# Kernel optimization log

Measured on AMD Instinct MI355X. Metric: run time of the kernel, lower is better.

## Reference

```python
import jax, jax.numpy as jnp
import numpy as np

EPS = 1e-8

def setup_inputs() -> dict:
    key = jax.random.key(0)
    ks = jax.random.split(key, 10)
    B, T, D = 128, 128, 512
    inp = {"joint": jax.random.normal(ks[0], (B, D), dtype=jnp.float32)}
    names = ["f00", "f01", "f02", "f10", "f11", "f12", "f20", "f21", "f22"]
    for n, k in zip(names, ks[1:]):
        inp[n] = jax.random.normal(k, (B, T, D), dtype=jnp.float32)
    inp["B"] = B
    return inp


def reference(joint, f00, f01, f02, f10, f11, f12, f20, f21, f22, B):
    # F: [N, N, B, T, D] with N = 3
    F = jnp.stack([
        jnp.stack([f00, f01, f02]),
        jnp.stack([f10, f11, f12]),
        jnp.stack([f20, f21, f22]),
    ])
    fmean = F.mean(axis=3)                                   # [N, N, B, D]
    num = jnp.einsum("bd,ijbd->ijb", joint, fmean)           # [N, N, B]
    denom = num.sum(axis=1, keepdims=True) + EPS             # [N, 1, B]
    b = num / denom                                          # [N, N, B]
    # intra-scale weighted sum: f_ii[i] = sum_j b[i,j] * F[i,j]
    f_ii = jnp.einsum("ijb,ijbtd->ibtd", b, F)               # [N, B, T, D]
    fii_mean = f_ii.mean(axis=2)                             # [N, B, D]
    num2 = jnp.einsum("bd,ibd->ib", joint, fii_mean)         # [N, B]
    denom2 = num2.sum(axis=0) + EPS                          # [B]
    lam = num2 / denom2                                      # [N, B]
    return jnp.einsum("ib,ibd->bd", lam, fii_mean)           # [B, D]
```

## Files before the change

### kernel.cpp

```cpp
#include <hip/hip_runtime.h>

#define EPS 1e-8f

namespace {
constexpr int Bc = 128;
constexpr int Tc = 128;
constexpr int Dc = 512;
constexpr int D4 = Dc / 4;
constexpr int THREADS = 256;
constexpr int BLOCKS_PER_TENSOR = (Bc * D4) / THREADS;
}

__global__ __launch_bounds__(256) void hm_mean_kernel(
    const float* __restrict__ f0, const float* __restrict__ f1,
    const float* __restrict__ f2, const float* __restrict__ f3,
    const float* __restrict__ f4, const float* __restrict__ f5,
    const float* __restrict__ f6, const float* __restrict__ f7,
    const float* __restrict__ f8, float* __restrict__ fmean)
{
    const float* fs[9] = {f0, f1, f2, f3, f4, f5, f6, f7, f8};
    const int q   = blockIdx.x / BLOCKS_PER_TENSOR;
    const int idx = (blockIdx.x % BLOCKS_PER_TENSOR) * THREADS + threadIdx.x;
    const int b   = idx >> 7;
    const int d4  = idx & (D4 - 1);

    const float4* src = reinterpret_cast<const float4*>(fs[q]) + (size_t)b * Tc * D4 + d4;

    float4 a0 = make_float4(0.f, 0.f, 0.f, 0.f);
    float4 a1 = make_float4(0.f, 0.f, 0.f, 0.f);
    #pragma unroll 8
    for (int t = 0; t < Tc; t += 2) {
        float4 v0 = src[(size_t)t * D4];
        float4 v1 = src[(size_t)(t + 1) * D4];
        a0.x += v0.x; a0.y += v0.y; a0.z += v0.z; a0.w += v0.w;
        a1.x += v1.x; a1.y += v1.y; a1.z += v1.z; a1.w += v1.w;
    }
    const float inv = 1.0f / (float)Tc;
    float4 r;
    r.x = (a0.x + a1.x) * inv;
    r.y = (a0.y + a1.y) * inv;
    r.z = (a0.z + a1.z) * inv;
    r.w = (a0.w + a1.w) * inv;
    reinterpret_cast<float4*>(fmean)[(size_t)q * Bc * D4 + idx] = r;
}

__global__ __launch_bounds__(256) void hm_final_kernel(
    const float* __restrict__ joint, const float* __restrict__ fmean,
    float* __restrict__ out)
{
    const int b   = blockIdx.x;
    const int tid = threadIdx.x;
    const int lane = tid & 63;
    const int wave = tid >> 6;

    __shared__ float sm_red[4][9];
    __shared__ float sm_red2[4][3];
    __shared__ float sm_num[9];
    __shared__ float sm_num2[3];

    float jd[2];
    float fm[2][9];
    float pnum[9];
    #pragma unroll
    for (int q = 0; q < 9; ++q) pnum[q] = 0.f;

    #pragma unroll
    for (int r = 0; r < 2; ++r) {
        const int d = tid + r * 256;
        jd[r] = joint[(size_t)b * Dc + d];
        #pragma unroll
        for (int q = 0; q < 9; ++q) {
            fm[r][q] = fmean[((size_t)q * Bc + b) * Dc + d];
            pnum[q] += jd[r] * fm[r][q];
        }
    }

    #pragma unroll
    for (int q = 0; q < 9; ++q)
        #pragma unroll
        for (int off = 32; off > 0; off >>= 1)
            pnum[q] += __shfl_down(pnum[q], off, 64);
    if (lane == 0)
        #pragma unroll
        for (int q = 0; q < 9; ++q) sm_red[wave][q] = pnum[q];
    __syncthreads();
    if (tid < 9)
        sm_num[tid] = sm_red[0][tid] + sm_red[1][tid] + sm_red[2][tid] + sm_red[3][tid];
    __syncthreads();

    float num[9];
    #pragma unroll
    for (int q = 0; q < 9; ++q) num[q] = sm_num[q];
    float bw[3][3];
    #pragma unroll
    for (int i = 0; i < 3; ++i) {
        const float denom = num[i * 3] + num[i * 3 + 1] + num[i * 3 + 2] + EPS;
        const float rdenom = 1.0f / denom;
        #pragma unroll
        for (int j = 0; j < 3; ++j) bw[i][j] = num[i * 3 + j] * rdenom;
    }

    float fii[2][3];
    float pnum2[3] = {0.f, 0.f, 0.f};
    #pragma unroll
    for (int r = 0; r < 2; ++r)
        #pragma unroll
        for (int i = 0; i < 3; ++i) {
            fii[r][i] = bw[i][0] * fm[r][i * 3 + 0]
                      + bw[i][1] * fm[r][i * 3 + 1]
                      + bw[i][2] * fm[r][i * 3 + 2];
            pnum2[i] += jd[r] * fii[r][i];
        }

    #pragma unroll
    for (int i = 0; i < 3; ++i)
        #pragma unroll
        for (int off = 32; off > 0; off >>= 1)
            pnum2[i] += __shfl_down(pnum2[i], off, 64);
    if (lane == 0)
        #pragma unroll
        for (int i = 0; i < 3; ++i) sm_red2[wave][i] = pnum2[i];
    __syncthreads();
    if (tid < 3)
        sm_num2[tid] = sm_red2[0][tid] + sm_red2[1][tid] + sm_red2[2][tid] + sm_red2[3][tid];
    __syncthreads();

    const float denom2 = sm_num2[0] + sm_num2[1] + sm_num2[2] + EPS;
    const float rd2 = 1.0f / denom2;
    float lam[3];
    #pragma unroll
    for (int i = 0; i < 3; ++i) lam[i] = sm_num2[i] * rd2;

    #pragma unroll
    for (int r = 0; r < 2; ++r) {
        const int d = tid + r * 256;
        out[(size_t)b * Dc + d] =
            lam[0] * fii[r][0] + lam[1] * fii[r][1] + lam[2] * fii[r][2];
    }
}

extern "C" void kernel_launch(void* const* d_in, const int* in_sizes, int n_in,
                              void* d_out, int out_size, void* d_ws, size_t ws_size,
                              hipStream_t stream) {
    const float* joint = (const float*)d_in[0];
    const float* f[9];
    for (int q = 0; q < 9; ++q) f[q] = (const float*)d_in[1 + q];
    float* out = (float*)d_out;
    float* fmean = (float*)d_ws;

    const int grid1 = 9 * BLOCKS_PER_TENSOR;
    hipLaunchKernelGGL(hm_mean_kernel, dim3(grid1), dim3(THREADS), 0, stream,
                       f[0], f[1], f[2], f[3], f[4], f[5], f[6], f[7], f[8], fmean);
    hipLaunchKernelGGL(hm_final_kernel, dim3(Bc), dim3(THREADS), 0, stream,
                       joint, fmean, out);
}
```

Before: 58.96 us.

## Split time axis into chunks to raise grid parallelism in mean kernel

The mean-reduction kernel now splits the T dimension into up to four chunks, each handled by separate blocks that write partial sums to workspace. The final kernel sums the partials and applies the 1/T scale. This increases the number of blocks in flight to better saturate memory bandwidth. The cost is extra workspace and more partial-sum reads in the final kernel, plus a runtime loop bound in the streaming loop.

```diff
diff --git a/kernel.cpp b/kernel.cpp
--- a/kernel.cpp
+++ b/kernel.cpp
@@ -16,40 +16,50 @@
     const float* __restrict__ f2, const float* __restrict__ f3,
     const float* __restrict__ f4, const float* __restrict__ f5,
     const float* __restrict__ f6, const float* __restrict__ f7,
-    const float* __restrict__ f8, float* __restrict__ fmean)
+    const float* __restrict__ f8, float* __restrict__ fpart,
+    int nch, int tpc)
 {
     const float* fs[9] = {f0, f1, f2, f3, f4, f5, f6, f7, f8};
-    const int q   = blockIdx.x / BLOCKS_PER_TENSOR;
-    const int idx = (blockIdx.x % BLOCKS_PER_TENSOR) * THREADS + threadIdx.x;
-    const int b   = idx >> 7;
-    const int d4  = idx & (D4 - 1);
+    const int bpt   = BLOCKS_PER_TENSOR * nch;
+    const int q     = blockIdx.x / bpt;
+    const int rest  = blockIdx.x % bpt;
+    const int chunk = rest / BLOCKS_PER_TENSOR;
+    const int blk   = rest % BLOCKS_PER_TENSOR;
+    const int idx   = blk * THREADS + threadIdx.x;
+    const int b     = idx >> 7;
+    const int d4    = idx & (D4 - 1);
 
-    const float4* src = reinterpret_cast<const float4*>(fs[q]) + (size_t)b * Tc * D4 + d4;
+    const float4* src = reinterpret_cast<const float4*>(fs[q])
+                      + (size_t)b * Tc * D4 + (size_t)chunk * tpc * D4 + d4;
 
     float4 a0 = make_float4(0.f, 0.f, 0.f, 0.f);
     float4 a1 = make_float4(0.f, 0.f, 0.f, 0.f);
-    #pragma unroll 8
-    for (int t = 0; t < Tc; t += 2) {
+    float4 a2 = make_float4(0.f, 0.f, 0.f, 0.f);
+    float4 a3 = make_float4(0.f, 0.f, 0.f, 0.f);
+    for (int t = 0; t < tpc; t += 4) {
         float4 v0 = src[(size_t)t * D4];
         float4 v1 = src[(size_t)(t + 1) * D4];
+        float4 v2 = src[(size_t)(t + 2) * D4];
+        float4 v3 = src[(size_t)(t + 3) * D4];
         a0.x += v0.x; a0.y += v0.y; a0.z += v0.z; a0.w += v0.w;
         a1.x += v1.x; a1.y += v1.y; a1.z += v1.z; a1.w += v1.w;
+        a2.x += v2.x; a2.y += v2.y; a2.z += v2.z; a2.w += v2.w;
+        a3.x += v3.x; a3.y += v3.y; a3.z += v3.z; a3.w += v3.w;
     }
-    const float inv = 1.0f / (float)Tc;
     float4 r;
-    r.x = (a0.x + a1.x) * inv;
-    r.y = (a0.y + a1.y) * inv;
-    r.z = (a0.z + a1.z) * inv;
-    r.w = (a0.w + a1.w) * inv;
-    reinterpret_cast<float4*>(fmean)[(size_t)q * Bc * D4 + idx] = r;
+    r.x = (a0.x + a1.x) + (a2.x + a3.x);
+    r.y = (a0.y + a1.y) + (a2.y + a3.y);
+    r.z = (a0.z + a1.z) + (a2.z + a3.z);
+    r.w = (a0.w + a1.w) + (a2.w + a3.w);
+    reinterpret_cast<float4*>(fpart)[(size_t)(chunk * 9 + q) * Bc * D4 + idx] = r;
 }
 
 __global__ __launch_bounds__(256) void hm_final_kernel(
-    const float* __restrict__ joint, const float* __restrict__ fmean,
-    float* __restrict__ out)
+    const float* __restrict__ joint, const float* __restrict__ fpart,
+    float* __restrict__ out, int nch)
 {
-    const int b   = blockIdx.x;
-    const int tid = threadIdx.x;
+    const int b    = blockIdx.x;
+    const int tid  = threadIdx.x;
     const int lane = tid & 63;
     const int wave = tid >> 6;
 
@@ -57,6 +67,8 @@
     __shared__ float sm_red2[4][3];
     __shared__ float sm_num[9];
     __shared__ float sm_num2[3];
+
+    const float invT = 1.0f / (float)Tc;
 
     float jd[2];
     float fm[2][9];
@@ -70,7 +82,10 @@
         jd[r] = joint[(size_t)b * Dc + d];
         #pragma unroll
         for (int q = 0; q < 9; ++q) {
-            fm[r][q] = fmean[((size_t)q * Bc + b) * Dc + d];
+            float s = 0.f;
+            for (int c = 0; c < nch; ++c)
+                s += fpart[((size_t)(c * 9 + q) * Bc + b) * Dc + d];
+            fm[r][q] = s * invT;
             pnum[q] += jd[r] * fm[r][q];
         }
     }
@@ -146,11 +161,17 @@
     const float* f[9];
     for (int q = 0; q < 9; ++q) f[q] = (const float*)d_in[1 + q];
     float* out = (float*)d_out;
-    float* fmean = (float*)d_ws;
+    float* fpart = (float*)d_ws;
 
-    const int grid1 = 9 * BLOCKS_PER_TENSOR;
+    const size_t plane = (size_t)9 * Bc * Dc * sizeof(float);
+    int nch = 4;
+    while (nch > 1 && (size_t)nch * plane > ws_size) nch >>= 1;
+    const int tpc = Tc / nch;
+
+    const int grid1 = 9 * BLOCKS_PER_TENSOR * nch;
     hipLaunchKernelGGL(hm_mean_kernel, dim3(grid1), dim3(THREADS), 0, stream,
-                       f[0], f[1], f[2], f[3], f[4], f[5], f[6], f[7], f[8], fmean);
+                       f[0], f[1], f[2], f[3], f[4], f[5], f[6], f[7], f[8],
+                       fpart, nch, tpc);
     hipLaunchKernelGGL(hm_final_kernel, dim3(Bc), dim3(THREADS), 0, stream,
-                       joint, fmean, out);
+                       joint, fpart, out, nch);
 }
```

Measured after the change: 77.74 us. 31.8% more time.
